# Kernel optimization log

Hardware: AMD Instinct MI355X
Metric: run time of the kernel (lower is better)

The kernel has to match this reference:

```python
import jax, jax.numpy as jnp
import numpy as np

C = 256
CI = C // 2  # inter_channels
EPS = 1e-5


def _proj(x, w, b):
    # 1x1 conv == channel matmul: w [O,C], x [n,c,h,w] -> [n,o,h,w]
    return jnp.einsum('oc,nchw->nohw', w, x) + b[None, :, None, None]


def setup_inputs() -> dict:
    key = jax.random.key(0)
    ks = jax.random.split(key, 12)
    shp = (4, C, 64, 64)
    s = 1.0 / np.sqrt(C)
    si = 1.0 / np.sqrt(CI)
    return {
        'x': jax.random.normal(ks[0], shp, jnp.float32),
        'y': jax.random.normal(ks[1], shp, jnp.float32),
        'theta_w': jax.random.normal(ks[2], (CI, C), jnp.float32) * s,
        'theta_b': jax.random.normal(ks[3], (CI,), jnp.float32) * s,
        'phi_w': jax.random.normal(ks[4], (CI, C), jnp.float32) * s,
        'phi_b': jax.random.normal(ks[5], (CI,), jnp.float32) * s,
        'g_w': jax.random.normal(ks[6], (CI, C), jnp.float32) * s,
        'g_b': jax.random.normal(ks[7], (CI,), jnp.float32) * s,
        'rec_w': jax.random.normal(ks[8], (C, CI), jnp.float32) * si,
        'rec_b': jax.random.normal(ks[9], (C,), jnp.float32) * si,
        'gamma': jnp.ones((C,), jnp.float32),
        'beta': jnp.zeros((C,), jnp.float32),
    }


def reference(x, y, theta_w, theta_b, phi_w, phi_b, g_w, g_b, rec_w, rec_b, gamma, beta):
    n, c, h, w = x.shape
    hw = h * w
    # projections (1x1 convs)
    g_x = _proj(x, g_w, g_b).reshape(n, CI, hw).transpose(0, 2, 1)        # [n,HW,CI]
    theta_x = _proj(x, theta_w, theta_b).reshape(n, CI, hw).transpose(0, 2, 1)  # [n,HW,CI]
    phi_y = _proj(y, phi_w, phi_b).reshape(n, CI, hw)                     # [n,CI,HW]
    # attention: QK^T -> softmax -> AV
    attn = jax.nn.softmax(jnp.einsum('nqc,nck->nqk', theta_x, phi_y), axis=-1)  # [n,HW,HW]
    out = jnp.einsum('nqk,nkc->nqc', attn, g_x)                           # [n,HW,CI]
    out = out.transpose(0, 2, 1).reshape(n, CI, h, w)
    out = _proj(out, rec_w, rec_b)                                        # [n,C,h,w]
    # BatchNorm2d (training-mode forward: batch stats over N,H,W; biased var)
    mean = out.mean(axis=(0, 2, 3))
    var = out.var(axis=(0, 2, 3))
    out = gamma[None, :, None, None] * (out - mean[None, :, None, None]) * jax.lax.rsqrt(var + EPS)[None, :, None, None] + beta[None, :, None, None]
    return x + out
```

## Files before the change

### kernel.cpp

```cpp
#include <hip/hip_runtime.h>
#include <math.h>

#define EPSV 1e-5f

typedef __attribute__((ext_vector_type(8))) _Float16 f16x8;
typedef __attribute__((ext_vector_type(4))) float f32x4;

typedef __attribute__((address_space(1))) const unsigned int as1_u32;
typedef __attribute__((address_space(3))) unsigned int as3_u32;

static __device__ __forceinline__ unsigned packh2(float a, float b) {
  auto v = __builtin_amdgcn_cvt_pkrtz(a, b);
  return __builtin_bit_cast(unsigned, v);
}

__global__ __launch_bounds__(256) void pack_w(const float* __restrict__ tw,
                                              const float* __restrict__ pw,
                                              const float* __restrict__ gw,
                                              const float* __restrict__ rw,
                                              _Float16* __restrict__ w16) {
  int i = blockIdx.x * 256 + threadIdx.x;
  const float* s = i < 32768 ? tw : (i < 65536 ? pw : (i < 98304 ? gw : rw));
  w16[i] = (_Float16)s[i & 32767];
}

__global__ __launch_bounds__(256) void pack_xy(const float* __restrict__ x,
                                               const float* __restrict__ y,
                                               _Float16* __restrict__ xt) {
  const int n = blockIdx.y, s = blockIdx.z;
  const int g = blockIdx.x * 256 + threadIdx.x;
  const int p = g & 4095, c8 = g >> 12;
  const float* src = (s ? y : x) + ((size_t)n * 256 + c8 * 8) * 4096 + p;
  f16x8 v;
#pragma unroll
  for (int j = 0; j < 8; ++j) v[j] = (_Float16)src[(size_t)j * 4096];
  *(f16x8*)(xt + ((size_t)(s * 4 + n) * 4096 + p) * 256 + c8 * 8) = v;
}

__global__ __launch_bounds__(256) void proj_kernel(
    const _Float16* __restrict__ xt, const _Float16* __restrict__ w16,
    const float* __restrict__ tb, const float* __restrict__ pb,
    const float* __restrict__ gb, _Float16* __restrict__ th16,
    _Float16* __restrict__ ph16, _Float16* __restrict__ g16) {
  const int ptile = blockIdx.x;
  const int z = blockIdx.y;
  const int pr = z >> 2, n = z & 3;
  const int p0 = ptile * 128;
  const int tid = threadIdx.x, wv = tid >> 6, lane = tid & 63, lg = lane >> 4, lr = lane & 15;

  __shared__ __align__(16) char sB[65536];

  const int srcn = (pr == 1 ? 4 : 0) + n;
  const char* src = (const char*)(xt + ((size_t)srcn * 4096 + p0) * 256);
#pragma unroll
  for (int ps = 0; ps < 16; ++ps) {
    int L = ps * 4096 + tid * 16;
    int row = L >> 9, col = L & 511;
    __builtin_amdgcn_global_load_lds((as1_u32*)(src + (size_t)row * 512 + (col ^ ((row & 7) << 4))),
                                     (as3_u32*)(sB + L), 16, 0, 0);
  }
  const _Float16* wp = w16 + pr * 32768;
  const float* bp = pr == 0 ? tb : (pr == 1 ? pb : gb);

  if (pr != 1) {
    const int o0 = wv * 32;
    f16x8 a[2][8];
#pragma unroll
    for (int mf = 0; mf < 2; ++mf)
#pragma unroll
      for (int kc = 0; kc < 8; ++kc)
        a[mf][kc] = *(const f16x8*)(wp + (size_t)(o0 + mf * 16 + lr) * 256 + kc * 32 + lg * 8);
    __syncthreads();
    f32x4 acc[2][8];
#pragma unroll
    for (int mf = 0; mf < 2; ++mf)
#pragma unroll
      for (int nf = 0; nf < 8; ++nf) acc[mf][nf] = f32x4{0.f, 0.f, 0.f, 0.f};
#pragma unroll
    for (int kc = 0; kc < 8; ++kc) {
      f16x8 bf[8];
#pragma unroll
      for (int nf = 0; nf < 8; ++nf)
        bf[nf] = *(const f16x8*)(sB + (nf * 16 + lr) * 512 + ((kc * 64 + lg * 16) ^ ((lr & 7) << 4)));
#pragma unroll
      for (int mf = 0; mf < 2; ++mf)
#pragma unroll
        for (int nf = 0; nf < 8; ++nf)
          acc[mf][nf] = __builtin_amdgcn_mfma_f32_16x16x32_f16(a[mf][kc], bf[nf], acc[mf][nf], 0, 0, 0);
    }
    _Float16* out = (pr == 0 ? th16 : g16) + (size_t)n * 128 * 4096;
#pragma unroll
    for (int mf = 0; mf < 2; ++mf)
#pragma unroll
      for (int r = 0; r < 4; ++r) {
        int o = o0 + mf * 16 + lg * 4 + r;
        float bias = bp[o];
#pragma unroll
        for (int nf = 0; nf < 8; ++nf)
          out[(size_t)o * 4096 + p0 + nf * 16 + lr] = (_Float16)(acc[mf][nf][r] + bias);
      }
  } else {
    __syncthreads();
    const int pw0 = wv * 32;
    f32x4 acc[2][8];
#pragma unroll
    for (int mf = 0; mf < 2; ++mf)
#pragma unroll
      for (int nf = 0; nf < 8; ++nf) acc[mf][nf] = f32x4{0.f, 0.f, 0.f, 0.f};
#pragma unroll 2
    for (int kc = 0; kc < 8; ++kc) {
      f16x8 bf[8];
#pragma unroll
      for (int nf = 0; nf < 8; ++nf)
        bf[nf] = *(const f16x8*)(wp + (size_t)(nf * 16 + lr) * 256 + kc * 32 + lg * 8);
      f16x8 af[2];
#pragma unroll
      for (int mf = 0; mf < 2; ++mf)
        af[mf] = *(const f16x8*)(sB + (pw0 + mf * 16 + lr) * 512 + ((kc * 64 + lg * 16) ^ ((lr & 7) << 4)));
#pragma unroll
      for (int mf = 0; mf < 2; ++mf)
#pragma unroll
        for (int nf = 0; nf < 8; ++nf)
          acc[mf][nf] = __builtin_amdgcn_mfma_f32_16x16x32_f16(af[mf], bf[nf], acc[mf][nf], 0, 0, 0);
    }
    _Float16* out = ph16 + (size_t)n * 4096 * 128;
#pragma unroll
    for (int mf = 0; mf < 2; ++mf)
#pragma unroll
      for (int r = 0; r < 4; ++r) {
        int p = p0 + pw0 + mf * 16 + lg * 4 + r;
#pragma unroll
        for (int nf = 0; nf < 8; ++nf) {
          int o = nf * 16 + lr;
          out[(size_t)p * 128 + o] = (_Float16)(acc[mf][nf][r] + bp[o]);
        }
      }
  }
}

__global__ __launch_bounds__(512) void attn_kernel(
    const _Float16* __restrict__ th16, const _Float16* __restrict__ ph16,
    const _Float16* __restrict__ g16, _Float16* __restrict__ o16) {
  const int lin = blockIdx.x;
  const int xcd = lin & 7;
  const int n = xcd >> 1;
  const int qt = ((lin >> 3) << 1) | (xcd & 1);
  const int q0 = qt * 64;
  const int tid = threadIdx.x;
  const int wv = tid >> 6, lane = tid & 63, lg = lane >> 4, lr = lane & 15;
  const int half = wv & 1, qsub = wv >> 1;

  __shared__ __align__(16) char smem[147456];
#define KBUF(h, b) (smem + ((h)*2 + (b)) * 16384)
#define GBUF(h, b) (smem + 65536 + ((h)*2 + (b)) * 16384)
  char* pB = smem + 131072 + wv * 2048;

  const _Float16* thn = th16 + (size_t)n * 128 * 4096;
  const char* phn = (const char*)(ph16 + (size_t)n * 4096 * 128);
  const char* ggn = (const char*)(g16 + (size_t)n * 128 * 4096);

  const char* ksrc = phn + (tid >> 4) * 256 + (((tid & 15) * 16) ^ (((tid >> 4) & 7) << 4));
  const char* gsrc = ggn + (size_t)(tid >> 3) * 8192 + (((tid & 7) * 16) ^ (((tid >> 3) & 7) << 4));

#define STAGE(KT, B)                                                                     \
  do {                                                                                   \
    _Pragma("unroll") for (int h_ = 0; h_ < 2; ++h_) {                                   \
      const char* ks = ksrc + (size_t)(h_ * 2048 + (KT) * 64) * 256;                     \
      const char* gs = gsrc + (size_t)(h_ * 2048 + (KT) * 64) * 2;                       \
      char* kd = KBUF(h_, B) + tid * 16;                                                 \
      char* gd = GBUF(h_, B) + tid * 16;                                                 \
      __builtin_amdgcn_global_load_lds((as1_u32*)ks, (as3_u32*)kd, 16, 0, 0);            \
      __builtin_amdgcn_global_load_lds((as1_u32*)(ks + 8192), (as3_u32*)(kd + 8192), 16, 0, 0); \
      __builtin_amdgcn_global_load_lds((as1_u32*)gs, (as3_u32*)gd, 16, 0, 0);            \
      __builtin_amdgcn_global_load_lds((as1_u32*)(gs + 524288), (as3_u32*)(gd + 8192), 16, 0, 0); \
    }                                                                                    \
  } while (0)

  const int q = q0 + qsub * 16 + lr;
  f16x8 qf[4];
#pragma unroll
  for (int ch = 0; ch < 4; ++ch)
#pragma unroll
    for (int j = 0; j < 8; ++j)
      qf[ch][j] = thn[(size_t)(ch * 32 + lg * 8 + j) * 4096 + q];

  const int swzk = (lr & 7) << 4;
  const int swzp = (lr & 15) << 3;

  f32x4 acc[8];
#pragma unroll
  for (int of = 0; of < 8; ++of) acc[of] = f32x4{0.f, 0.f, 0.f, 0.f};
  float mrow = -INFINITY, lrow = 0.f;

  STAGE(0, 0);
  __syncthreads();

  for (int kt = 0; kt < 32; ++kt) {
    const int b = kt & 1;
    if (kt < 31) STAGE(kt + 1, b ^ 1);

    const char* kb = KBUF(half, b);
    f32x4 s[4];
    __builtin_amdgcn_s_setprio(1);
#pragma unroll
    for (int cf = 0; cf < 4; ++cf) {
      const char* krow = kb + (cf * 16 + lr) * 256;
      f32x4 sv = f32x4{0.f, 0.f, 0.f, 0.f};
#pragma unroll
      for (int ch = 0; ch < 4; ++ch) {
        f16x8 kf = *(const f16x8*)(krow + ((ch * 64 + lg * 16) ^ swzk));
        sv = __builtin_amdgcn_mfma_f32_16x16x32_f16(kf, qf[ch], sv, 0, 0, 0);
      }
      s[cf] = sv;
    }
    __builtin_amdgcn_s_setprio(0);

    float mt = s[0][0];
#pragma unroll
    for (int cf = 0; cf < 4; ++cf)
#pragma unroll
      for (int r = 0; r < 4; ++r) mt = fmaxf(mt, s[cf][r]);
    mt = fmaxf(mt, __shfl_xor(mt, 16));
    mt = fmaxf(mt, __shfl_xor(mt, 32));
    if (!__all(mt <= mrow + 8.0f)) {
      float mnew = fmaxf(mrow, mt);
      float sc = __expf(mrow - mnew);
#pragma unroll
      for (int of = 0; of < 8; ++of) acc[of] *= sc;
      lrow *= sc;
      mrow = mnew;
    }
    float psum = 0.f;
    char* prow = pB + lr * 128;
#pragma unroll
    for (int cf = 0; cf < 4; ++cf) {
      float p0 = __expf(s[cf][0] - mrow);
      float p1 = __expf(s[cf][1] - mrow);
      float p2 = __expf(s[cf][2] - mrow);
      float p3 = __expf(s[cf][3] - mrow);
      psum += (p0 + p1) + (p2 + p3);
      unsigned long long w = (unsigned long long)packh2(p0, p1) |
                             ((unsigned long long)packh2(p2, p3) << 32);
      *(unsigned long long*)(prow + ((cf * 32 + lg * 8) ^ swzp)) = w;
    }
    psum += __shfl_xor(psum, 16);
    psum += __shfl_xor(psum, 32);
    lrow += psum;

    const char* gb = GBUF(half, b);
    __builtin_amdgcn_s_setprio(1);
#pragma unroll
    for (int kc = 0; kc < 2; ++kc) {
      int b0 = kc * 64 + lg * 16;
      unsigned long long w0 = *(const unsigned long long*)(prow + (b0 ^ swzp));
      unsigned long long w1 = *(const unsigned long long*)(prow + ((b0 + 8) ^ swzp));
      f16x8 pf;
      unsigned* pu = (unsigned*)&pf;
      pu[0] = (unsigned)w0; pu[1] = (unsigned)(w0 >> 32);
      pu[2] = (unsigned)w1; pu[3] = (unsigned)(w1 >> 32);
#pragma unroll
      for (int of = 0; of < 8; ++of) {
        f16x8 gf = *(const f16x8*)(gb + (of * 16 + lr) * 128 + ((kc * 64 + lg * 16) ^ swzk));
        acc[of] = __builtin_amdgcn_mfma_f32_16x16x32_f16(gf, pf, acc[of], 0, 0, 0);
      }
    }
    __builtin_amdgcn_s_setprio(0);
    __syncthreads();
  }

  float* mg = (float*)(smem + qsub * 9216);
  if (half == 1) {
#pragma unroll
    for (int of = 0; of < 8; ++of)
#pragma unroll
      for (int r = 0; r < 4; ++r) mg[lane * 36 + of * 4 + r] = acc[of][r];
    mg[lane * 36 + 32] = mrow;
    mg[lane * 36 + 33] = lrow;
  }
  __syncthreads();
  if (half == 0) {
    float pm = mg[lane * 36 + 32];
    float pl = mg[lane * 36 + 33];
    float mm = fmaxf(mrow, pm);
    float a0 = __expf(mrow - mm), a1 = __expf(pm - mm);
    float inv = 1.0f / (lrow * a0 + pl * a1);
#pragma unroll
    for (int of = 0; of < 8; ++of)
#pragma unroll
      for (int r = 0; r < 4; ++r)
        acc[of][r] = (acc[of][r] * a0 + mg[lane * 36 + of * 4 + r] * a1) * inv;
  }
  __syncthreads();
  if (half == 0) {
    float* ep = (float*)(smem + qsub * 8448);
#pragma unroll
    for (int of = 0; of < 8; ++of)
#pragma unroll
      for (int r = 0; r < 4; ++r) ep[lr * 132 + of * 16 + lg * 4 + r] = acc[of][r];
    char* on = (char*)(o16 + (size_t)n * 4096 * 128);
#pragma unroll
    for (int it = 0; it < 4; ++it) {
      int e = lane + it * 64;
      int qq = e >> 4, c8 = e & 15;
      f32x4 va = *(const f32x4*)(ep + qq * 132 + c8 * 8);
      f32x4 vb = *(const f32x4*)(ep + qq * 132 + c8 * 8 + 4);
      f16x8 h;
#pragma unroll
      for (int j = 0; j < 4; ++j) { h[j] = (_Float16)va[j]; h[4 + j] = (_Float16)vb[j]; }
      *(f16x8*)(on + (size_t)(q0 + qsub * 16 + qq) * 256 + c8 * 16) = h;
    }
  }
#undef STAGE
#undef KBUF
#undef GBUF
}

__global__ __launch_bounds__(256) void rec_kernel(
    const _Float16* __restrict__ o16, const _Float16* __restrict__ rw16,
    const float* __restrict__ rb, float* __restrict__ out,
    float* __restrict__ partial) {
  const int pblk = blockIdx.x;
  const int n = blockIdx.y;
  const int p0 = pblk * 32;
  const int blin = n * 128 + pblk;
  const int tid = threadIdx.x, wv = tid >> 6, lane = tid & 63, lg = lane >> 4, lr = lane & 15;
  __shared__ __align__(16) char sB[8192];
  const char* o16n = (const char*)(o16 + (size_t)n * 4096 * 128);
  const char* srcb = o16n + (size_t)p0 * 256 + (tid >> 4) * 256 +
                     (((tid & 15) * 16) ^ (((tid >> 4) & 7) << 4));
  __builtin_amdgcn_global_load_lds((as1_u32*)srcb, (as3_u32*)(sB + tid * 16), 16, 0, 0);
  __builtin_amdgcn_global_load_lds((as1_u32*)(srcb + 4096), (as3_u32*)(sB + 4096 + tid * 16), 16, 0, 0);

  const int wc0 = wv * 64;
  f16x8 a[4][4];
#pragma unroll
  for (int mf = 0; mf < 4; ++mf)
#pragma unroll
    for (int kc = 0; kc < 4; ++kc)
      a[mf][kc] = *(const f16x8*)(rw16 + (size_t)(wc0 + mf * 16 + lr) * 128 + kc * 32 + lg * 8);
  __syncthreads();

  f32x4 acc[4][2];
#pragma unroll
  for (int mf = 0; mf < 4; ++mf) {
    acc[mf][0] = f32x4{0.f, 0.f, 0.f, 0.f};
    acc[mf][1] = f32x4{0.f, 0.f, 0.f, 0.f};
  }
  const int xorv = (lr & 7) << 4;
#pragma unroll
  for (int kc = 0; kc < 4; ++kc) {
    int cb = (kc * 64 + lg * 16) ^ xorv;
    f16x8 b0 = *(const f16x8*)(sB + lr * 256 + cb);
    f16x8 b1 = *(const f16x8*)(sB + (16 + lr) * 256 + cb);
#pragma unroll
    for (int mf = 0; mf < 4; ++mf) {
      acc[mf][0] = __builtin_amdgcn_mfma_f32_16x16x32_f16(a[mf][kc], b0, acc[mf][0], 0, 0, 0);
      acc[mf][1] = __builtin_amdgcn_mfma_f32_16x16x32_f16(a[mf][kc], b1, acc[mf][1], 0, 0, 0);
    }
  }
  float* pslot = partial + (size_t)blin * 512;
#pragma unroll
  for (int mf = 0; mf < 4; ++mf)
#pragma unroll
    for (int r = 0; r < 4; ++r) {
      int c = wc0 + mf * 16 + lg * 4 + r;
      float bias = rb[c];
      float v0 = acc[mf][0][r] + bias;
      float v1 = acc[mf][1][r] + bias;
      out[((size_t)n * 256 + c) * 4096 + p0 + lr] = v0;
      out[((size_t)n * 256 + c) * 4096 + p0 + 16 + lr] = v1;
      float s = v0 + v1, qd = v0 * v0 + v1 * v1;
      s += __shfl_xor(s, 1); qd += __shfl_xor(qd, 1);
      s += __shfl_xor(s, 2); qd += __shfl_xor(qd, 2);
      s += __shfl_xor(s, 4); qd += __shfl_xor(qd, 4);
      s += __shfl_xor(s, 8); qd += __shfl_xor(qd, 8);
      if (lr == 0) {
        pslot[c] = s;
        pslot[256 + c] = qd;
      }
    }
}

__global__ __launch_bounds__(256) void stats_reduce(const float* __restrict__ partial,
                                                    float* __restrict__ stats) {
  const int j = blockIdx.x * 256 + threadIdx.x;
  float s = 0.f;
#pragma unroll 8
  for (int b = 0; b < 512; ++b) s += partial[(size_t)b * 512 + j];
  stats[j] = s;
}

__global__ __launch_bounds__(256) void bn_kernel(
    const float* __restrict__ x, const float* __restrict__ gamma,
    const float* __restrict__ beta, const float* __restrict__ stats,
    float* __restrict__ out) {
  const size_t i4 = (size_t)blockIdx.x * 256 + threadIdx.x;
  const int c = (int)((i4 >> 10) & 255);
  const float inv = 1.f / 16384.f;
  const float mean = stats[c] * inv;
  const float var = stats[256 + c] * inv - mean * mean;
  const float gm = gamma[c] * rsqrtf(var + EPSV);
  const float bt = beta[c];
  float4 rv = ((const float4*)out)[i4];
  float4 xv = ((const float4*)x)[i4];
  float4 o;
  o.x = xv.x + (rv.x - mean) * gm + bt;
  o.y = xv.y + (rv.y - mean) * gm + bt;
  o.z = xv.z + (rv.z - mean) * gm + bt;
  o.w = xv.w + (rv.w - mean) * gm + bt;
  ((float4*)out)[i4] = o;
}

extern "C" void kernel_launch(void* const* d_in, const int* in_sizes, int n_in,
                              void* d_out, int out_size, void* d_ws, size_t ws_size,
                              hipStream_t stream) {
  const float* x  = (const float*)d_in[0];
  const float* y  = (const float*)d_in[1];
  const float* tw = (const float*)d_in[2];
  const float* tb = (const float*)d_in[3];
  const float* pw = (const float*)d_in[4];
  const float* pb = (const float*)d_in[5];
  const float* gw = (const float*)d_in[6];
  const float* gb = (const float*)d_in[7];
  const float* rw = (const float*)d_in[8];
  const float* rb = (const float*)d_in[9];
  const float* gamma = (const float*)d_in[10];
  const float* beta  = (const float*)d_in[11];
  float* out = (float*)d_out;
  _Float16* xt   = (_Float16*)d_ws;
  _Float16* w16  = xt + 8388608;
  _Float16* th16 = w16 + 131072;
  _Float16* ph16 = th16 + 2097152;
  _Float16* g16  = ph16 + 2097152;
  _Float16* o16  = g16 + 2097152;
  float* partial = (float*)(o16 + 2097152);
  float* stats   = partial + 262144;
  _Float16* rw16 = w16 + 98304;
  pack_w<<<dim3(512), 256, 0, stream>>>(tw, pw, gw, rw, w16);
  pack_xy<<<dim3(512, 4, 2), 256, 0, stream>>>(x, y, xt);
  proj_kernel<<<dim3(32, 12), 256, 0, stream>>>(xt, w16, tb, pb, gb, th16, ph16, g16);
  attn_kernel<<<dim3(256), 512, 0, stream>>>(th16, ph16, g16, o16);
  rec_kernel<<<dim3(128, 4), 256, 0, stream>>>(o16, rw16, rb, out, partial);
  stats_reduce<<<dim3(2), 256, 0, stream>>>(partial, stats);
  bn_kernel<<<dim3(4096), 256, 0, stream>>>(x, gamma, beta, stats, out);
}
```

Measured before the change: 139.6 us.

## Split attention KV across blocks with separate merge kernel, fp16 rec intermediate

Attention now splits the key/value range across two independent 256-thread blocks per query tile and writes fp32 partial outputs plus row max/sum. A new merge kernel combines them in place of the in-block LDS merge. This halves shared memory per block so two blocks fit per CU. Theta is now written in row-major [p,c] layout so query fragments load as vectors. The reconstruction output is stored as fp16 in a new buffer, and BN reads it, which cuts intermediate traffic. The cost is an extra launch, a partial-output round trip, and fp16 rounding of the pre-BN values.

New measurement: 145.1 us. +3.9%, slower.

```diff
diff --git a/kernel.cpp b/kernel.cpp
--- a/kernel.cpp
+++ b/kernel.cpp
@@ -4,6 +4,7 @@
 #define EPSV 1e-5f
 
 typedef __attribute__((ext_vector_type(8))) _Float16 f16x8;
+typedef __attribute__((ext_vector_type(4))) _Float16 f16x4;
 typedef __attribute__((ext_vector_type(4))) float f32x4;
 
 typedef __attribute__((address_space(1))) const unsigned int as1_u32;
@@ -62,7 +63,7 @@
   const _Float16* wp = w16 + pr * 32768;
   const float* bp = pr == 0 ? tb : (pr == 1 ? pb : gb);
 
-  if (pr != 1) {
+  if (pr == 2) {
     const int o0 = wv * 32;
     f16x8 a[2][8];
 #pragma unroll
@@ -88,7 +89,7 @@
         for (int nf = 0; nf < 8; ++nf)
           acc[mf][nf] = __builtin_amdgcn_mfma_f32_16x16x32_f16(a[mf][kc], bf[nf], acc[mf][nf], 0, 0, 0);
     }
-    _Float16* out = (pr == 0 ? th16 : g16) + (size_t)n * 128 * 4096;
+    _Float16* out = g16 + (size_t)n * 128 * 4096;
 #pragma unroll
     for (int mf = 0; mf < 2; ++mf)
 #pragma unroll
@@ -123,7 +124,7 @@
         for (int nf = 0; nf < 8; ++nf)
           acc[mf][nf] = __builtin_amdgcn_mfma_f32_16x16x32_f16(af[mf], bf[nf], acc[mf][nf], 0, 0, 0);
     }
-    _Float16* out = ph16 + (size_t)n * 4096 * 128;
+    _Float16* out = (pr == 0 ? th16 : ph16) + (size_t)n * 4096 * 128;
 #pragma unroll
     for (int mf = 0; mf < 2; ++mf)
 #pragma unroll
@@ -138,51 +139,52 @@
   }
 }
 
-__global__ __launch_bounds__(512) void attn_kernel(
+__global__ __launch_bounds__(256, 2) void attn_kernel(
     const _Float16* __restrict__ th16, const _Float16* __restrict__ ph16,
-    const _Float16* __restrict__ g16, _Float16* __restrict__ o16) {
+    const _Float16* __restrict__ g16, float* __restrict__ po,
+    float2* __restrict__ ml) {
   const int lin = blockIdx.x;
   const int xcd = lin & 7;
   const int n = xcd >> 1;
-  const int qt = ((lin >> 3) << 1) | (xcd & 1);
+  const int kvh = xcd & 1;
+  const int qt = lin >> 3;
   const int q0 = qt * 64;
   const int tid = threadIdx.x;
   const int wv = tid >> 6, lane = tid & 63, lg = lane >> 4, lr = lane & 15;
-  const int half = wv & 1, qsub = wv >> 1;
-
-  __shared__ __align__(16) char smem[147456];
-#define KBUF(h, b) (smem + ((h)*2 + (b)) * 16384)
-#define GBUF(h, b) (smem + 65536 + ((h)*2 + (b)) * 16384)
-  char* pB = smem + 131072 + wv * 2048;
-
-  const _Float16* thn = th16 + (size_t)n * 128 * 4096;
+  const int kv0 = kvh * 2048;
+
+  __shared__ __align__(16) char smem[73728];
+#define KBUF(B) (smem + (B) * 16384)
+#define GBUF(B) (smem + 32768 + (B) * 16384)
+  char* pB = smem + 65536 + wv * 2048;
+
+  const _Float16* thn = th16 + (size_t)n * 4096 * 128;
   const char* phn = (const char*)(ph16 + (size_t)n * 4096 * 128);
   const char* ggn = (const char*)(g16 + (size_t)n * 128 * 4096);
 
-  const char* ksrc = phn + (tid >> 4) * 256 + (((tid & 15) * 16) ^ (((tid >> 4) & 7) << 4));
-  const char* gsrc = ggn + (size_t)(tid >> 3) * 8192 + (((tid & 7) * 16) ^ (((tid >> 3) & 7) << 4));
+  const char* ksrc = phn + (size_t)kv0 * 256 + (tid >> 4) * 256 +
+                     (((tid & 15) * 16) ^ (((tid >> 4) & 7) << 4));
+  const char* gsrc = ggn + (size_t)(tid >> 3) * 8192 + kv0 * 2 +
+                     (((tid & 7) * 16) ^ (((tid >> 3) & 7) << 4));
 
 #define STAGE(KT, B)                                                                     \
   do {                                                                                   \
-    _Pragma("unroll") for (int h_ = 0; h_ < 2; ++h_) {                                   \
-      const char* ks = ksrc + (size_t)(h_ * 2048 + (KT) * 64) * 256;                     \
-      const char* gs = gsrc + (size_t)(h_ * 2048 + (KT) * 64) * 2;                       \
-      char* kd = KBUF(h_, B) + tid * 16;                                                 \
-      char* gd = GBUF(h_, B) + tid * 16;                                                 \
-      __builtin_amdgcn_global_load_lds((as1_u32*)ks, (as3_u32*)kd, 16, 0, 0);            \
-      __builtin_amdgcn_global_load_lds((as1_u32*)(ks + 8192), (as3_u32*)(kd + 8192), 16, 0, 0); \
-      __builtin_amdgcn_global_load_lds((as1_u32*)gs, (as3_u32*)gd, 16, 0, 0);            \
-      __builtin_amdgcn_global_load_lds((as1_u32*)(gs + 524288), (as3_u32*)(gd + 8192), 16, 0, 0); \
+    const char* ks = ksrc + (size_t)(KT) * 16384;                                        \
+    const char* gs = gsrc + (size_t)(KT) * 128;                                          \
+    char* kd = KBUF(B) + tid * 16;                                                       \
+    char* gd = GBUF(B) + tid * 16;                                                       \
+    _Pragma("unroll") for (int i_ = 0; i_ < 4; ++i_) {                                   \
+      __builtin_amdgcn_global_load_lds((as1_u32*)(ks + i_ * 4096),                       \
+                                       (as3_u32*)(kd + i_ * 4096), 16, 0, 0);            \
+      __builtin_amdgcn_global_load_lds((as1_u32*)(gs + (size_t)i_ * 262144),             \
+                                       (as3_u32*)(gd + i_ * 4096), 16, 0, 0);            \
     }                                                                                    \
   } while (0)
 
-  const int q = q0 + qsub * 16 + lr;
   f16x8 qf[4];
 #pragma unroll
   for (int ch = 0; ch < 4; ++ch)
-#pragma unroll
-    for (int j = 0; j < 8; ++j)
-      qf[ch][j] = thn[(size_t)(ch * 32 + lg * 8 + j) * 4096 + q];
+    qf[ch] = *(const f16x8*)(thn + (size_t)(q0 + wv * 16 + lr) * 128 + ch * 32 + lg * 8);
 
   const int swzk = (lr & 7) << 4;
   const int swzp = (lr & 15) << 3;
@@ -199,7 +201,7 @@
     const int b = kt & 1;
     if (kt < 31) STAGE(kt + 1, b ^ 1);
 
-    const char* kb = KBUF(half, b);
+    const char* kb = KBUF(b);
     f32x4 s[4];
     __builtin_amdgcn_s_setprio(1);
 #pragma unroll
@@ -247,13 +249,13 @@
     psum += __shfl_xor(psum, 32);
     lrow += psum;
 
-    const char* gb = GBUF(half, b);
+    const char* gb = GBUF(b);
     __builtin_amdgcn_s_setprio(1);
 #pragma unroll
     for (int kc = 0; kc < 2; ++kc) {
-      int b0 = kc * 64 + lg * 16;
-      unsigned long long w0 = *(const unsigned long long*)(prow + (b0 ^ swzp));
-      unsigned long long w1 = *(const unsigned long long*)(prow + ((b0 + 8) ^ swzp));
+      const int b0 = kc * 64 + lg * 16;
+      unsigned long long w0 = *(unsigned long long*)(prow + (b0 ^ swzp));
+      unsigned long long w1 = *(unsigned long long*)(prow + ((b0 + 8) ^ swzp));
       f16x8 pf;
       unsigned* pu = (unsigned*)&pf;
       pu[0] = (unsigned)w0; pu[1] = (unsigned)(w0 >> 32);
@@ -268,56 +270,57 @@
     __syncthreads();
   }
 
-  float* mg = (float*)(smem + qsub * 9216);
-  if (half == 1) {
-#pragma unroll
-    for (int of = 0; of < 8; ++of)
-#pragma unroll
-      for (int r = 0; r < 4; ++r) mg[lane * 36 + of * 4 + r] = acc[of][r];
-    mg[lane * 36 + 32] = mrow;
-    mg[lane * 36 + 33] = lrow;
-  }
   __syncthreads();
-  if (half == 0) {
-    float pm = mg[lane * 36 + 32];
-    float pl = mg[lane * 36 + 33];
-    float mm = fmaxf(mrow, pm);
-    float a0 = __expf(mrow - mm), a1 = __expf(pm - mm);
-    float inv = 1.0f / (lrow * a0 + pl * a1);
-#pragma unroll
-    for (int of = 0; of < 8; ++of)
-#pragma unroll
-      for (int r = 0; r < 4; ++r)
-        acc[of][r] = (acc[of][r] * a0 + mg[lane * 36 + of * 4 + r] * a1) * inv;
-  }
-  __syncthreads();
-  if (half == 0) {
-    float* ep = (float*)(smem + qsub * 8448);
-#pragma unroll
-    for (int of = 0; of < 8; ++of)
-#pragma unroll
-      for (int r = 0; r < 4; ++r) ep[lr * 132 + of * 16 + lg * 4 + r] = acc[of][r];
-    char* on = (char*)(o16 + (size_t)n * 4096 * 128);
-#pragma unroll
-    for (int it = 0; it < 4; ++it) {
-      int e = lane + it * 64;
-      int qq = e >> 4, c8 = e & 15;
-      f32x4 va = *(const f32x4*)(ep + qq * 132 + c8 * 8);
-      f32x4 vb = *(const f32x4*)(ep + qq * 132 + c8 * 8 + 4);
-      f16x8 h;
-#pragma unroll
-      for (int j = 0; j < 4; ++j) { h[j] = (_Float16)va[j]; h[4 + j] = (_Float16)vb[j]; }
-      *(f16x8*)(on + (size_t)(q0 + qsub * 16 + qq) * 256 + c8 * 16) = h;
-    }
-  }
+  float* ep = (float*)(smem + wv * 8448);
+#pragma unroll
+  for (int of = 0; of < 8; ++of)
+#pragma unroll
+    for (int r = 0; r < 4; ++r) ep[lr * 132 + of * 16 + lg * 4 + r] = acc[of][r];
+  float* pon = po + ((size_t)(kvh * 4 + n) * 4096 + q0 + wv * 16) * 128;
+#pragma unroll
+  for (int it = 0; it < 8; ++it) {
+    int e = lane + it * 64;
+    int qq = e >> 5, c4 = e & 31;
+    *(f32x4*)(pon + (size_t)qq * 128 + c4 * 4) = *(const f32x4*)(ep + qq * 132 + c4 * 4);
+  }
+  if (lg == 0) ml[(size_t)(kvh * 4 + n) * 4096 + q0 + wv * 16 + lr] = float2{mrow, lrow};
 #undef STAGE
 #undef KBUF
 #undef GBUF
 }
 
+__global__ __launch_bounds__(256) void merge_kernel(const float* __restrict__ po,
+                                                    const float2* __restrict__ ml,
+                                                    _Float16* __restrict__ o16) {
+  const int t = threadIdx.x;
+  const int row = blockIdx.x * 32 + (t >> 3);
+  const int c0 = (t & 7) * 16;
+  const float2 a = ml[row], b = ml[16384 + row];
+  const float M = fmaxf(a.x, b.x);
+  const float fa = __expf(a.x - M), fb = __expf(b.x - M);
+  const float inv = 1.0f / (a.y * fa + b.y * fb);
+  const float* pa = po + (size_t)row * 128 + c0;
+  const float* pb2 = po + (size_t)(16384 + row) * 128 + c0;
+  _Float16* out = o16 + (size_t)row * 128 + c0;
+#pragma unroll
+  for (int h = 0; h < 2; ++h) {
+    f32x4 va0 = *(const f32x4*)(pa + h * 8);
+    f32x4 va1 = *(const f32x4*)(pa + h * 8 + 4);
+    f32x4 vb0 = *(const f32x4*)(pb2 + h * 8);
+    f32x4 vb1 = *(const f32x4*)(pb2 + h * 8 + 4);
+    f16x8 o;
+#pragma unroll
+    for (int j = 0; j < 4; ++j) {
+      o[j] = (_Float16)((va0[j] * fa + vb0[j] * fb) * inv);
+      o[4 + j] = (_Float16)((va1[j] * fa + vb1[j] * fb) * inv);
+    }
+    *(f16x8*)(out + h * 8) = o;
+  }
+}
+
 __global__ __launch_bounds__(256) void rec_kernel(
     const _Float16* __restrict__ o16, const _Float16* __restrict__ rw16,
-    const float* __restrict__ rb, float* __restrict__ out,
+    const float* __restrict__ rb, _Float16* __restrict__ rec16,
     float* __restrict__ partial) {
   const int pblk = blockIdx.x;
   const int n = blockIdx.y;
@@ -367,8 +370,8 @@
       float bias = rb[c];
       float v0 = acc[mf][0][r] + bias;
       float v1 = acc[mf][1][r] + bias;
-      out[((size_t)n * 256 + c) * 4096 + p0 + lr] = v0;
-      out[((size_t)n * 256 + c) * 4096 + p0 + 16 + lr] = v1;
+      rec16[((size_t)n * 256 + c) * 4096 + p0 + lr] = (_Float16)v0;
+      rec16[((size_t)n * 256 + c) * 4096 + p0 + 16 + lr] = (_Float16)v1;
       float s = v0 + v1, qd = v0 * v0 + v1 * v1;
       s += __shfl_xor(s, 1); qd += __shfl_xor(qd, 1);
       s += __shfl_xor(s, 2); qd += __shfl_xor(qd, 2);
@@ -393,7 +396,7 @@
 __global__ __launch_bounds__(256) void bn_kernel(
     const float* __restrict__ x, const float* __restrict__ gamma,
     const float* __restrict__ beta, const float* __restrict__ stats,
-    float* __restrict__ out) {
+    const _Float16* __restrict__ rec16, float* __restrict__ out) {
   const size_t i4 = (size_t)blockIdx.x * 256 + threadIdx.x;
   const int c = (int)((i4 >> 10) & 255);
   const float inv = 1.f / 16384.f;
@@ -401,13 +404,13 @@
   const float var = stats[256 + c] * inv - mean * mean;
   const float gm = gamma[c] * rsqrtf(var + EPSV);
   const float bt = beta[c];
-  float4 rv = ((const float4*)out)[i4];
+  f16x4 r4 = ((const f16x4*)rec16)[i4];
   float4 xv = ((const float4*)x)[i4];
   float4 o;
-  o.x = xv.x + (rv.x - mean) * gm + bt;
-  o.y = xv.y + (rv.y - mean) * gm + bt;
-  o.z = xv.z + (rv.z - mean) * gm + bt;
-  o.w = xv.w + (rv.w - mean) * gm + bt;
+  o.x = xv.x + ((float)r4[0] - mean) * gm + bt;
+  o.y = xv.y + ((float)r4[1] - mean) * gm + bt;
+  o.z = xv.z + ((float)r4[2] - mean) * gm + bt;
+  o.w = xv.w + ((float)r4[3] - mean) * gm + bt;
   ((float4*)out)[i4] = o;
 }
 
@@ -427,20 +430,24 @@
   const float* gamma = (const float*)d_in[10];
   const float* beta  = (const float*)d_in[11];
   float* out = (float*)d_out;
-  _Float16* xt   = (_Float16*)d_ws;
-  _Float16* w16  = xt + 8388608;
-  _Float16* th16 = w16 + 131072;
-  _Float16* ph16 = th16 + 2097152;
-  _Float16* g16  = ph16 + 2097152;
-  _Float16* o16  = g16 + 2097152;
-  float* partial = (float*)(o16 + 2097152);
-  float* stats   = partial + 262144;
+  _Float16* xt    = (_Float16*)d_ws;
+  _Float16* w16   = xt + 8388608;
+  _Float16* th16  = w16 + 131072;
+  _Float16* ph16  = th16 + 2097152;
+  _Float16* g16   = ph16 + 2097152;
+  _Float16* o16   = g16 + 2097152;
+  _Float16* rec16 = o16 + 2097152;
+  float* partial  = (float*)(rec16 + 4194304);
+  float* stats    = partial + 262144;
+  float2* ml      = (float2*)(stats + 512);
+  float* po       = (float*)xt;
   _Float16* rw16 = w16 + 98304;
   pack_w<<<dim3(512), 256, 0, stream>>>(tw, pw, gw, rw, w16);
   pack_xy<<<dim3(512, 4, 2), 256, 0, stream>>>(x, y, xt);
   proj_kernel<<<dim3(32, 12), 256, 0, stream>>>(xt, w16, tb, pb, gb, th16, ph16, g16);
-  attn_kernel<<<dim3(256), 512, 0, stream>>>(th16, ph16, g16, o16);
-  rec_kernel<<<dim3(128, 4), 256, 0, stream>>>(o16, rw16, rb, out, partial);
+  attn_kernel<<<dim3(512), 256, 0, stream>>>(th16, ph16, g16, po, ml);
+  merge_kernel<<<dim3(512), 256, 0, stream>>>(po, ml, o16);
+  rec_kernel<<<dim3(128, 4), 256, 0, stream>>>(o16, rw16, rb, rec16, partial);
   stats_reduce<<<dim3(2), 256, 0, stream>>>(partial, stats);
-  bn_kernel<<<dim3(4096), 256, 0, stream>>>(x, gamma, beta, stats, out);
-}
+  bn_kernel<<<dim3(4096), 256, 0, stream>>>(x, gamma, beta, stats, rec16, out);
+}
```
